# Optimization experiments

Measured on AMD Instinct MI355X. Metric: run time of the kernel, lower is better.

Reference implementation:

```python
import jax, jax.numpy as jnp
import numpy as np

B, IN, H, OUT = 32, 128, 1024, 128  # batch, input(charset), hidden, output(charset)


def setup_inputs() -> dict:
    key = jax.random.key(0)
    ks = jax.random.split(key, 10)
    scale = 0.02  # small fast-weight init (candidate_weights start at zero and accumulate)
    d = {}
    d["x"] = jax.random.normal(ks[0], (B, IN), jnp.float32)
    d["hidden"] = jax.random.normal(ks[1], (B, H), jnp.float32)
    # Per-sample dynamic (fast) weight matrices: candidate_weights of each HebbianLinear,
    # shape [batch_size, out_features, in_features] as in the torch module.
    d["W0"] = jax.random.normal(ks[2], (B, H, IN + H), jnp.float32) * scale  # layer 0: (in+hid)->hid
    d["b0"] = jnp.zeros((H,), jnp.float32)
    d["W1"] = jax.random.normal(ks[3], (B, H, H), jnp.float32) * scale      # layer 1
    d["b1"] = jnp.zeros((H,), jnp.float32)
    d["W2"] = jax.random.normal(ks[4], (B, H, H), jnp.float32) * scale      # layer 2
    d["b2"] = jnp.zeros((H,), jnp.float32)
    d["Wh"] = jax.random.normal(ks[5], (B, H, H), jnp.float32) * scale      # i2h head
    d["bh"] = jnp.zeros((H,), jnp.float32)
    d["Wo"] = jax.random.normal(ks[6], (B, OUT, H), jnp.float32) * scale    # i2o head (is_last_layer)
    d["bo"] = jnp.zeros((OUT,), jnp.float32)
    return d


def _hebbian_linear(W, b, x):
    # torch: torch.bmm(candidate_weights, input.unsqueeze(2)).squeeze(2) + bias
    return jnp.einsum('boi,bi->bo', W, x) + b


def reference(x, hidden, W0, b0, W1, b1, W2, b2, Wh, bh, Wo, bo):
    # combined = cat(input, hidden); stack of HebbianLinear layers with tanh nonlinearity
    combined = jnp.concatenate([x, hidden], axis=1)          # [B, IN+H]
    combined = jnp.tanh(_hebbian_linear(W0, b0, combined))   # [B, H]
    combined = jnp.tanh(_hebbian_linear(W1, b1, combined))
    combined = jnp.tanh(_hebbian_linear(W2, b2, combined))
    # dropout is identity in eval mode
    new_hidden = jnp.tanh(_hebbian_linear(Wh, bh, combined))  # [B, H]
    logits = _hebbian_linear(Wo, bo, combined)                # [B, OUT]
    output = jax.nn.log_softmax(logits, axis=1)
    return output, new_hidden
```

## Files before the change

### kernel.cpp

```cpp
#include <hip/hip_runtime.h>
#include <math.h>


#define B_SZ 32
#define IN_SZ 128
#define H_SZ 1024
#define OUT_SZ 128

__global__ void concat_kernel(const float* __restrict__ x,
                              const float* __restrict__ h,
                              float* __restrict__ out) {
    int tid = blockIdx.x * blockDim.x + threadIdx.x;
    if (tid < B_SZ * (IN_SZ + H_SZ)) {
        int b = tid / (IN_SZ + H_SZ);
        int i = tid - b * (IN_SZ + H_SZ);
        out[tid] = (i < IN_SZ) ? x[b * IN_SZ + i] : h[b * H_SZ + (i - IN_SZ)];
    }
}

__global__ void gemv_kernel(const float* __restrict__ W,
                            const float* __restrict__ bias,
                            const float* __restrict__ v,
                            float* __restrict__ out,
                            int O, int I, int applyTanh) {
    int wave = blockIdx.x * (blockDim.x >> 6) + (threadIdx.x >> 6);
    int lane = threadIdx.x & 63;
    int row = wave;
    int b = row / O;
    int o = row - b * O;

    const float4* __restrict__ Wr = (const float4*)(W + (size_t)row * I);
    const float4* __restrict__ vr = (const float4*)(v + (size_t)b * I);
    int n4 = I >> 2;

    float sum = 0.f;
    for (int j = lane; j < n4; j += 64) {
        float4 w4 = Wr[j];
        float4 a4 = vr[j];
        sum += w4.x * a4.x + w4.y * a4.y + w4.z * a4.z + w4.w * a4.w;
    }
    #pragma unroll
    for (int off = 32; off > 0; off >>= 1)
        sum += __shfl_down(sum, off, 64);

    if (lane == 0) {
        float r = sum + bias[o];
        out[row] = applyTanh ? tanhf(r) : r;
    }
}

__global__ void logsoftmax_kernel(const float* __restrict__ logits,
                                  float* __restrict__ out) {
    int b = blockIdx.x;
    int lane = threadIdx.x;
    float v0 = logits[b * OUT_SZ + lane];
    float v1 = logits[b * OUT_SZ + 64 + lane];
    float m = fmaxf(v0, v1);
    #pragma unroll
    for (int off = 32; off > 0; off >>= 1)
        m = fmaxf(m, __shfl_xor(m, off, 64));
    float e = __expf(v0 - m) + __expf(v1 - m);
    #pragma unroll
    for (int off = 32; off > 0; off >>= 1)
        e += __shfl_xor(e, off, 64);
    float lse = m + logf(e);
    out[b * OUT_SZ + lane]      = v0 - lse;
    out[b * OUT_SZ + 64 + lane] = v1 - lse;
}

extern "C" void kernel_launch(void* const* d_in, const int* in_sizes, int n_in,
                              void* d_out, int out_size, void* d_ws, size_t ws_size,
                              hipStream_t stream) {
    const float* x      = (const float*)d_in[0];
    const float* hidden = (const float*)d_in[1];
    const float* W0 = (const float*)d_in[2];
    const float* b0 = (const float*)d_in[3];
    const float* W1 = (const float*)d_in[4];
    const float* b1 = (const float*)d_in[5];
    const float* W2 = (const float*)d_in[6];
    const float* b2 = (const float*)d_in[7];
    const float* Wh = (const float*)d_in[8];
    const float* bh = (const float*)d_in[9];
    const float* Wo = (const float*)d_in[10];
    const float* bo = (const float*)d_in[11];

    float* out_ls     = (float*)d_out;
    float* new_hidden = out_ls + B_SZ * OUT_SZ;

    float* ws = (float*)d_ws;
    float* combined = ws;
    float* c1 = combined + B_SZ * (IN_SZ + H_SZ);
    float* c2 = c1 + B_SZ * H_SZ;
    float* logits = c2 + B_SZ * H_SZ;

    concat_kernel<<<(B_SZ * (IN_SZ + H_SZ) + 255) / 256, 256, 0, stream>>>(
        x, hidden, combined);

    const int blocksH = (B_SZ * H_SZ) / 4;
    gemv_kernel<<<blocksH, 256, 0, stream>>>(W0, b0, combined, c1, H_SZ, IN_SZ + H_SZ, 1);
    gemv_kernel<<<blocksH, 256, 0, stream>>>(W1, b1, c1, c2, H_SZ, H_SZ, 1);
    gemv_kernel<<<blocksH, 256, 0, stream>>>(W2, b2, c2, c1, H_SZ, H_SZ, 1);
    gemv_kernel<<<blocksH, 256, 0, stream>>>(Wh, bh, c1, new_hidden, H_SZ, H_SZ, 1);

    gemv_kernel<<<(B_SZ * OUT_SZ) / 4, 256, 0, stream>>>(Wo, bo, c1, logits, OUT_SZ, H_SZ, 0);

    logsoftmax_kernel<<<B_SZ, 64, 0, stream>>>(logits, out_ls);
}
```

Measured before the change: 483.5 us.

## Fuse concat into first GEMV, merge head GEMVs, fully unroll fixed-size loops

Drops the separate concat kernel by having the first layer's GEMV read x and hidden directly. The i2h and i2o head GEMVs are merged into a single launch. All GEMVs are specialized to compile-time sizes with fully unrolled float4 loads, so each lane issues several independent loads at once. This removes two launches and an extra round trip through global memory for the concatenated input. It also adds a little branching in the head kernel.

```diff
diff --git a/kernel.cpp b/kernel.cpp
--- a/kernel.cpp
+++ b/kernel.cpp
@@ -7,45 +7,103 @@
 #define H_SZ 1024
 #define OUT_SZ 128
 
-__global__ void concat_kernel(const float* __restrict__ x,
-                              const float* __restrict__ h,
-                              float* __restrict__ out) {
-    int tid = blockIdx.x * blockDim.x + threadIdx.x;
-    if (tid < B_SZ * (IN_SZ + H_SZ)) {
-        int b = tid / (IN_SZ + H_SZ);
-        int i = tid - b * (IN_SZ + H_SZ);
-        out[tid] = (i < IN_SZ) ? x[b * IN_SZ + i] : h[b * H_SZ + (i - IN_SZ)];
-    }
+__device__ __forceinline__ float wave_reduce(float s) {
+    #pragma unroll
+    for (int off = 32; off > 0; off >>= 1)
+        s += __shfl_down(s, off, 64);
+    return s;
 }
 
-__global__ void gemv_kernel(const float* __restrict__ W,
-                            const float* __restrict__ bias,
-                            const float* __restrict__ v,
-                            float* __restrict__ out,
-                            int O, int I, int applyTanh) {
-    int wave = blockIdx.x * (blockDim.x >> 6) + (threadIdx.x >> 6);
+__device__ __forceinline__ float dot4(float4 w, float4 a) {
+    return w.x * a.x + w.y * a.y + w.z * a.z + w.w * a.w;
+}
+
+__global__ void gemv0_kernel(const float* __restrict__ W,
+                             const float* __restrict__ bias,
+                             const float* __restrict__ x,
+                             const float* __restrict__ h,
+                             float* __restrict__ out) {
+    int wave = blockIdx.x * 4 + (threadIdx.x >> 6);
     int lane = threadIdx.x & 63;
-    int row = wave;
-    int b = row / O;
-    int o = row - b * O;
+    int b = wave >> 10;
+    int o = wave & 1023;
 
-    const float4* __restrict__ Wr = (const float4*)(W + (size_t)row * I);
-    const float4* __restrict__ vr = (const float4*)(v + (size_t)b * I);
-    int n4 = I >> 2;
+    const float4* __restrict__ Wr = (const float4*)(W + (size_t)wave * (IN_SZ + H_SZ));
+    const float4* __restrict__ x4 = (const float4*)(x + b * IN_SZ);
+    const float4* __restrict__ h4 = (const float4*)(h + b * H_SZ);
 
     float sum = 0.f;
-    for (int j = lane; j < n4; j += 64) {
-        float4 w4 = Wr[j];
-        float4 a4 = vr[j];
-        sum += w4.x * a4.x + w4.y * a4.y + w4.z * a4.z + w4.w * a4.w;
+    #pragma unroll
+    for (int k = 0; k < 4; k++) {
+        int j = lane + 64 * k;
+        float4 w = Wr[j];
+        float4 a = (j < 32) ? x4[j] : h4[j - 32];
+        sum += dot4(w, a);
     }
+    if (lane < 32) {
+        int j = 256 + lane;
+        float4 w = Wr[j];
+        float4 a = h4[j - 32];
+        sum += dot4(w, a);
+    }
+    sum = wave_reduce(sum);
+    if (lane == 0) out[wave] = tanhf(sum + bias[o]);
+}
+
+__global__ void gemv_mid_kernel(const float* __restrict__ W,
+                                const float* __restrict__ bias,
+                                const float* __restrict__ v,
+                                float* __restrict__ out) {
+    int wave = blockIdx.x * 4 + (threadIdx.x >> 6);
+    int lane = threadIdx.x & 63;
+    int b = wave >> 10;
+    int o = wave & 1023;
+
+    const float4* __restrict__ Wr = (const float4*)(W + (size_t)wave * H_SZ);
+    const float4* __restrict__ vr = (const float4*)(v + b * H_SZ);
+
+    float sum = 0.f;
     #pragma unroll
-    for (int off = 32; off > 0; off >>= 1)
-        sum += __shfl_down(sum, off, 64);
+    for (int k = 0; k < 4; k++) {
+        int j = lane + 64 * k;
+        sum += dot4(Wr[j], vr[j]);
+    }
+    sum = wave_reduce(sum);
+    if (lane == 0) out[wave] = tanhf(sum + bias[o]);
+}
 
+__global__ void heads_kernel(const float* __restrict__ Wh,
+                             const float* __restrict__ bh,
+                             const float* __restrict__ Wo,
+                             const float* __restrict__ bo,
+                             const float* __restrict__ v,
+                             float* __restrict__ new_hidden,
+                             float* __restrict__ logits) {
+    int wave = blockIdx.x * 4 + (threadIdx.x >> 6);
+    int lane = threadIdx.x & 63;
+    bool isO = wave >= B_SZ * H_SZ;
+    int r = isO ? wave - B_SZ * H_SZ : wave;
+    int b = isO ? (r >> 7) : (r >> 10);
+
+    const float* Wbase = isO ? (Wo + (size_t)r * H_SZ) : (Wh + (size_t)r * H_SZ);
+    const float4* __restrict__ Wr = (const float4*)Wbase;
+    const float4* __restrict__ vr = (const float4*)(v + b * H_SZ);
+
+    float sum = 0.f;
+    #pragma unroll
+    for (int k = 0; k < 4; k++) {
+        int j = lane + 64 * k;
+        sum += dot4(Wr[j], vr[j]);
+    }
+    sum = wave_reduce(sum);
     if (lane == 0) {
-        float r = sum + bias[o];
-        out[row] = applyTanh ? tanhf(r) : r;
+        if (isO) {
+            int o = r & (OUT_SZ - 1);
+            logits[r] = sum + bo[o];
+        } else {
+            int o = r & (H_SZ - 1);
+            new_hidden[r] = tanhf(sum + bh[o]);
+        }
     }
 }
 
@@ -88,21 +146,17 @@
     float* new_hidden = out_ls + B_SZ * OUT_SZ;
 
     float* ws = (float*)d_ws;
-    float* combined = ws;
-    float* c1 = combined + B_SZ * (IN_SZ + H_SZ);
+    float* c1 = ws;
     float* c2 = c1 + B_SZ * H_SZ;
     float* logits = c2 + B_SZ * H_SZ;
 
-    concat_kernel<<<(B_SZ * (IN_SZ + H_SZ) + 255) / 256, 256, 0, stream>>>(
-        x, hidden, combined);
+    const int blocksH = (B_SZ * H_SZ) / 4;
+    gemv0_kernel<<<blocksH, 256, 0, stream>>>(W0, b0, x, hidden, c1);
+    gemv_mid_kernel<<<blocksH, 256, 0, stream>>>(W1, b1, c1, c2);
+    gemv_mid_kernel<<<blocksH, 256, 0, stream>>>(W2, b2, c2, c1);
 
-    const int blocksH = (B_SZ * H_SZ) / 4;
-    gemv_kernel<<<blocksH, 256, 0, stream>>>(W0, b0, combined, c1, H_SZ, IN_SZ + H_SZ, 1);
-    gemv_kernel<<<blocksH, 256, 0, stream>>>(W1, b1, c1, c2, H_SZ, H_SZ, 1);
-    gemv_kernel<<<blocksH, 256, 0, stream>>>(W2, b2, c2, c1, H_SZ, H_SZ, 1);
-    gemv_kernel<<<blocksH, 256, 0, stream>>>(Wh, bh, c1, new_hidden, H_SZ, H_SZ, 1);
-
-    gemv_kernel<<<(B_SZ * OUT_SZ) / 4, 256, 0, stream>>>(Wo, bo, c1, logits, OUT_SZ, H_SZ, 0);
+    const int blocksHeads = (B_SZ * H_SZ + B_SZ * OUT_SZ) / 4;
+    heads_kernel<<<blocksHeads, 256, 0, stream>>>(Wh, bh, Wo, bo, c1, new_hidden, logits);
 
     logsoftmax_kernel<<<B_SZ, 64, 0, stream>>>(logits, out_ls);
 }
```

After: 460.9 us. 1.05x faster.
